# Optimization experiments

Measured on AMD Instinct MI355X. Metric: run time of the kernel, lower is better.

Reference implementation:

```python
import jax, jax.numpy as jnp
import numpy as np

B = 4096          # batch_size per view
D = 256           # projection feature dim
TEMP_F = 0.5      # temperature_f


def setup_inputs() -> dict:
    key = jax.random.key(0)
    k1, k2 = jax.random.split(key)
    return {
        "h_i": jax.random.normal(k1, (B, D), dtype=jnp.float32),
        "h_j": jax.random.normal(k2, (B, D), dtype=jnp.float32),
    }


def reference(h_i, h_j):
    # NT-Xent contrastive loss (forward_feature).
    batch = h_i.shape[0]
    N = 2 * batch
    h = jnp.concatenate([h_i, h_j], axis=0)                 # [N, D]
    sim = (h @ h.T) / TEMP_F                                # [N, N]

    # positives: sim(i, i+batch) and sim(i+batch, i)
    sim_i_j = jnp.diagonal(sim, offset=batch)               # [batch]
    sim_j_i = jnp.diagonal(sim, offset=-batch)              # [batch]
    pos = jnp.concatenate([sim_i_j, sim_j_i], axis=0)       # [N]

    # Torch builds logits = [pos_i, negatives_i] per row where negatives are
    # sim[i, :] with the diagonal AND the positive-pair entry removed, then
    # takes CE with label 0. Since the removed positive-pair entry equals
    # pos_i itself, logsumexp(logits_i) == logsumexp(sim[i, :] with only the
    # diagonal masked). So: loss_i = logsumexp(sim_masked[i]) - pos_i.
    neg_inf = jnp.finfo(sim.dtype).min
    eye = jnp.eye(N, dtype=bool)
    sim_masked = jnp.where(eye, neg_inf, sim)               # mask self-similarity
    lse = jax.nn.logsumexp(sim_masked, axis=1)              # [N]

    # CrossEntropyLoss(reduction='sum') / N  == mean over rows
    loss = jnp.mean(lse - pos)
    return loss
```

## Files before the change

kernel.cpp:

```cpp
#include <hip/hip_runtime.h>
#include <hip/hip_bf16.h>
#include <stdint.h>

#define BATCH 4096
#define N_TOT 8192
#define D_DIM 256
#define SHIFT 150.0f
#define SQRT2 1.41421356237309515f

typedef __bf16 bf16_t;
typedef bf16_t bf16x8 __attribute__((ext_vector_type(8)));
typedef bf16_t bf16x4 __attribute__((ext_vector_type(4)));
typedef float f32x4 __attribute__((ext_vector_type(4)));

__device__ __forceinline__ void gl_lds16(const void* g, void* l) {
  __builtin_amdgcn_global_load_lds(
      (const __attribute__((address_space(1))) void*)(uintptr_t)g,
      (__attribute__((address_space(3))) void*)(uint32_t)(uintptr_t)l,
      16, 0, 0);
}

__global__ void k_prep(const float* __restrict__ hi, const float* __restrict__ hj,
                       bf16_t* __restrict__ hb, float* __restrict__ Zrow,
                       float* __restrict__ posPartial) {
  const int wave = threadIdx.x >> 6, lane = threadIdx.x & 63;
  const int r = blockIdx.x * 4 + wave;
  const size_t off = (size_t)r * D_DIM + lane * 4;
  float4 a = *(const float4*)(hi + off);
  float4 b = *(const float4*)(hj + off);

  bf16x4 oa, ob;
  oa[0] = (bf16_t)(a.x * SQRT2); oa[1] = (bf16_t)(a.y * SQRT2);
  oa[2] = (bf16_t)(a.z * SQRT2); oa[3] = (bf16_t)(a.w * SQRT2);
  ob[0] = (bf16_t)(b.x * SQRT2); ob[1] = (bf16_t)(b.y * SQRT2);
  ob[2] = (bf16_t)(b.z * SQRT2); ob[3] = (bf16_t)(b.w * SQRT2);
  *(bf16x4*)(hb + off) = oa;
  *(bf16x4*)(hb + (size_t)BATCH * D_DIM + off) = ob;

  float d = a.x * b.x + a.y * b.y + a.z * b.z + a.w * b.w;
#pragma unroll
  for (int o = 32; o >= 1; o >>= 1) d += __shfl_xor(d, o);
  __shared__ float ps[4];
  if (lane == 0) ps[wave] = d;
  if (threadIdx.x < 8) Zrow[blockIdx.x * 8 + threadIdx.x] = 0.f;
  __syncthreads();
  if (threadIdx.x == 0) posPartial[blockIdx.x] = ps[0] + ps[1] + ps[2] + ps[3];
}

__global__ __launch_bounds__(256, 4) void k_gemm(const bf16_t* __restrict__ hb,
                                                 float* __restrict__ Zrow) {
  const int t = blockIdx.x;
  int bj = (int)((sqrtf(8.0f * (float)t + 1.0f) - 1.0f) * 0.5f);
  while ((bj + 1) * (bj + 2) / 2 <= t) ++bj;
  while (bj * (bj + 1) / 2 > t) --bj;
  const int bi = t - bj * (bj + 1) / 2;
  const int rBase = bi * 128;
  const int cBase = bj * 128;
  const bool diag = (bi == bj);

  __shared__ __align__(16) bf16_t As[128][64];
  __shared__ __align__(16) bf16_t Bs[128][64];
  const int tid = threadIdx.x;
  const int lane = tid & 63;
  const int wave = tid >> 6;

  const int half = wave & 1;
  const size_t stageRow = (size_t)((wave < 2 ? rBase : cBase) + half * 64);
  const int c_src = (lane & 7) ^ (lane >> 3);
  const bf16_t* gsrc = hb + stageRow * D_DIM + (size_t)(lane >> 3) * D_DIM + c_src * 8;
  bf16_t* lbase = (wave < 2) ? &As[half * 64][0] : &Bs[half * 64][0];

  const int wm = wave >> 1, wn = wave & 1;
  const int quad = lane >> 4, l16 = lane & 15;
  const int sw = l16 & 7;

  f32x4 acc[4][4];
#pragma unroll
  for (int i = 0; i < 4; ++i)
#pragma unroll
    for (int j = 0; j < 4; ++j) acc[i][j] = (f32x4){0.f, 0.f, 0.f, 0.f};

#pragma unroll
  for (int kc = 0; kc < 4; ++kc) {
    __syncthreads();
#pragma unroll
    for (int i = 0; i < 8; ++i)
      gl_lds16(gsrc + (size_t)i * 8 * D_DIM + kc * 64, lbase + i * 8 * 64);
    __syncthreads();
#pragma unroll
    for (int ks = 0; ks < 2; ++ks) {
      bf16x8 af[4], bfr[4];
      const int chunk = ((ks * 4 + quad) ^ sw) * 8;
#pragma unroll
      for (int mt = 0; mt < 4; ++mt)
        af[mt] = *(const bf16x8*)&As[wm * 64 + mt * 16 + l16][chunk];
#pragma unroll
      for (int nt = 0; nt < 4; ++nt)
        bfr[nt] = *(const bf16x8*)&Bs[wn * 64 + nt * 16 + l16][chunk];
#pragma unroll
      for (int mt = 0; mt < 4; ++mt)
#pragma unroll
        for (int nt = 0; nt < 4; ++nt)
          acc[mt][nt] = __builtin_amdgcn_mfma_f32_16x16x32_bf16(af[mt], bfr[nt],
                                                                acc[mt][nt], 0, 0, 0);
    }
  }

  const int rW = rBase + wm * 64 + quad * 4;
  const int cW = cBase + wn * 64 + l16;
  float colAcc[4] = {0.f, 0.f, 0.f, 0.f};
#pragma unroll
  for (int mt = 0; mt < 4; ++mt) {
#pragma unroll
    for (int rg = 0; rg < 4; ++rg) {
      const int rr = rW + mt * 16 + rg;
      float s = 0.f;
#pragma unroll
      for (int nt = 0; nt < 4; ++nt) {
        float e = __expf(acc[mt][nt][rg] - SHIFT);
        if (diag && (rr == cW + nt * 16)) e = 0.f;
        s += e;
        colAcc[nt] += e;
      }
      s += __shfl_xor(s, 1);
      s += __shfl_xor(s, 2);
      s += __shfl_xor(s, 4);
      s += __shfl_xor(s, 8);
      if (l16 == 0) atomicAdd(&Zrow[rr], s);
    }
  }
  if (!diag) {
#pragma unroll
    for (int nt = 0; nt < 4; ++nt) {
      float c = colAcc[nt];
      c += __shfl_xor(c, 16);
      c += __shfl_xor(c, 32);
      if (lane < 16) atomicAdd(&Zrow[cW + nt * 16], c);
    }
  }
}

__global__ void k_finish(const float* __restrict__ Zrow,
                         const float* __restrict__ posPartial,
                         float* __restrict__ out) {
  const int t = threadIdx.x;
  float4 z0 = *(const float4*)(Zrow + t * 8);
  float4 z1 = *(const float4*)(Zrow + t * 8 + 4);
  float sl = __logf(z0.x) + __logf(z0.y) + __logf(z0.z) + __logf(z0.w) +
             __logf(z1.x) + __logf(z1.y) + __logf(z1.z) + __logf(z1.w);
  float sp = posPartial[t];
#pragma unroll
  for (int o = 32; o >= 1; o >>= 1) {
    sl += __shfl_xor(sl, o);
    sp += __shfl_xor(sp, o);
  }
  __shared__ float pl[16], pp[16];
  const int wave = t >> 6, lane = t & 63;
  if (lane == 0) { pl[wave] = sl; pp[wave] = sp; }
  __syncthreads();
  if (t == 0) {
    float L = 0.f, P = 0.f;
    for (int i = 0; i < 16; ++i) { L += pl[i]; P += pp[i]; }
    out[0] = L / (float)N_TOT + SHIFT - P / 2048.0f;
  }
}

extern "C" void kernel_launch(void* const* d_in, const int* in_sizes, int n_in,
                              void* d_out, int out_size, void* d_ws, size_t ws_size,
                              hipStream_t stream) {
  const float* hi = (const float*)d_in[0];
  const float* hj = (const float*)d_in[1];
  float* out = (float*)d_out;

  bf16_t* hb = (bf16_t*)d_ws;
  float* Zrow = (float*)((char*)d_ws + (size_t)N_TOT * D_DIM * 2);
  float* posPartial = Zrow + N_TOT;

  k_prep<<<1024, 256, 0, stream>>>(hi, hj, hb, Zrow, posPartial);
  k_gemm<<<2080, 256, 0, stream>>>(hb, Zrow);
  k_finish<<<1, 1024, 0, stream>>>(Zrow, posPartial, out);
}
```

Measured before the change: 96.59 us.

## Double-buffer LDS tiles to overlap global loads with MFMA compute

Doubles the A/B LDS tiles and prefetches the next K-chunk into the alternate buffer while the current one is consumed, using manual vmcnt waits and raw barriers in place of paired __syncthreads. All fragments of a chunk are loaded before the MFMA burst, with a sched_barrier between. Launch bounds drop from 4 to 2 blocks per SM to allow more registers. Occupancy falls because of the doubled LDS (64KB per block) and the larger register budget, which may offset the latency hiding for a loop of only four K-chunks.

Result: slower. 103.2 us (+6.8%).

```diff
diff --git a/kernel.cpp b/kernel.cpp
--- a/kernel.cpp
+++ b/kernel.cpp
@@ -47,7 +47,7 @@
   if (threadIdx.x == 0) posPartial[blockIdx.x] = ps[0] + ps[1] + ps[2] + ps[3];
 }
 
-__global__ __launch_bounds__(256, 4) void k_gemm(const bf16_t* __restrict__ hb,
+__global__ __launch_bounds__(256, 2) void k_gemm(const bf16_t* __restrict__ hb,
                                                  float* __restrict__ Zrow) {
   const int t = blockIdx.x;
   int bj = (int)((sqrtf(8.0f * (float)t + 1.0f) - 1.0f) * 0.5f);
@@ -58,8 +58,8 @@
   const int cBase = bj * 128;
   const bool diag = (bi == bj);
 
-  __shared__ __align__(16) bf16_t As[128][64];
-  __shared__ __align__(16) bf16_t Bs[128][64];
+  __shared__ __align__(16) bf16_t As[2][128][64];
+  __shared__ __align__(16) bf16_t Bs[2][128][64];
   const int tid = threadIdx.x;
   const int lane = tid & 63;
   const int wave = tid >> 6;
@@ -68,7 +68,14 @@
   const size_t stageRow = (size_t)((wave < 2 ? rBase : cBase) + half * 64);
   const int c_src = (lane & 7) ^ (lane >> 3);
   const bf16_t* gsrc = hb + stageRow * D_DIM + (size_t)(lane >> 3) * D_DIM + c_src * 8;
-  bf16_t* lbase = (wave < 2) ? &As[half * 64][0] : &Bs[half * 64][0];
+  bf16_t* lbase = (wave < 2) ? &As[0][half * 64][0] : &Bs[0][half * 64][0];
+
+  auto STAGE = [&](int s, int b) {
+#pragma unroll
+    for (int i = 0; i < 8; ++i)
+      gl_lds16(gsrc + (size_t)i * 8 * D_DIM + s * 64,
+               lbase + b * (128 * 64) + i * 8 * 64);
+  };
 
   const int wm = wave >> 1, wn = wave & 1;
   const int quad = lane >> 4, l16 = lane & 15;
@@ -80,30 +87,43 @@
 #pragma unroll
     for (int j = 0; j < 4; ++j) acc[i][j] = (f32x4){0.f, 0.f, 0.f, 0.f};
 
-#pragma unroll
-  for (int kc = 0; kc < 4; ++kc) {
-    __syncthreads();
-#pragma unroll
-    for (int i = 0; i < 8; ++i)
-      gl_lds16(gsrc + (size_t)i * 8 * D_DIM + kc * 64, lbase + i * 8 * 64);
-    __syncthreads();
+  STAGE(0, 0);
+
+#pragma unroll
+  for (int k = 0; k < 4; ++k) {
+    const int b = k & 1;
+    if (k + 1 < 4) {
+      STAGE(k + 1, b ^ 1);
+      asm volatile("s_waitcnt vmcnt(8)" ::: "memory");
+    } else {
+      asm volatile("s_waitcnt vmcnt(0)" ::: "memory");
+    }
+    __builtin_amdgcn_s_barrier();
+
+    bf16x8 af[2][4], bfr[2][4];
 #pragma unroll
     for (int ks = 0; ks < 2; ++ks) {
-      bf16x8 af[4], bfr[4];
       const int chunk = ((ks * 4 + quad) ^ sw) * 8;
 #pragma unroll
       for (int mt = 0; mt < 4; ++mt)
-        af[mt] = *(const bf16x8*)&As[wm * 64 + mt * 16 + l16][chunk];
+        af[ks][mt] = *(const bf16x8*)&As[b][wm * 64 + mt * 16 + l16][chunk];
 #pragma unroll
       for (int nt = 0; nt < 4; ++nt)
-        bfr[nt] = *(const bf16x8*)&Bs[wn * 64 + nt * 16 + l16][chunk];
+        bfr[ks][nt] = *(const bf16x8*)&Bs[b][wn * 64 + nt * 16 + l16][chunk];
+    }
+    asm volatile("s_waitcnt lgkmcnt(0)" ::: "memory");
+    __builtin_amdgcn_sched_barrier(0);
+
+#pragma unroll
+    for (int ks = 0; ks < 2; ++ks)
 #pragma unroll
       for (int mt = 0; mt < 4; ++mt)
 #pragma unroll
         for (int nt = 0; nt < 4; ++nt)
-          acc[mt][nt] = __builtin_amdgcn_mfma_f32_16x16x32_bf16(af[mt], bfr[nt],
-                                                                acc[mt][nt], 0, 0, 0);
-    }
+          acc[mt][nt] = __builtin_amdgcn_mfma_f32_16x16x32_bf16(
+              af[ks][mt], bfr[ks][nt], acc[mt][nt], 0, 0, 0);
+
+    __builtin_amdgcn_s_barrier();
   }
 
   const int rW = rBase + wm * 64 + quad * 4;
```

## Drop LDS staging: plane-major bf16 layout with per-wave 64x64 tiles and register double-buffering

Applied to the files above, without the earlier changes.

The prep kernel now writes the bf16 features in a plane-major layout (8-element k-chunks per plane), so each lane can load MFMA fragments straight from global memory with coalesced 16-byte loads. The GEMM drops shared memory and block-wide barriers: each wave owns its own 64x64 upper-triangular tile and double-buffers fragments in registers, ordering the loads with manual vmcnt waits and scheduling fences. This removes LDS traffic and __syncthreads stalls, but every wave re-reads its operands from global/L2 with no reuse across waves, and the launch bound drops to 3 blocks per SIMD to make room for the extra registers.

After: 97.80 us. No clear change (+1.3%).

```diff
diff --git a/kernel.cpp b/kernel.cpp
--- a/kernel.cpp
+++ b/kernel.cpp
@@ -7,21 +7,19 @@
 #define D_DIM 256
 #define SHIFT 150.0f
 #define SQRT2 1.41421356237309515f
+#define NWTILE 8256
+#define PLANE 8192
 
 typedef __bf16 bf16_t;
 typedef bf16_t bf16x8 __attribute__((ext_vector_type(8)));
 typedef bf16_t bf16x4 __attribute__((ext_vector_type(4)));
 typedef float f32x4 __attribute__((ext_vector_type(4)));
 
-__device__ __forceinline__ void gl_lds16(const void* g, void* l) {
-  __builtin_amdgcn_global_load_lds(
-      (const __attribute__((address_space(1))) void*)(uintptr_t)g,
-      (__attribute__((address_space(3))) void*)(uint32_t)(uintptr_t)l,
-      16, 0, 0);
-}
+#define VMCNT(N) asm volatile("s_waitcnt vmcnt(" #N ")" ::: "memory")
+#define SCHED_FENCE() __builtin_amdgcn_sched_barrier(0)
 
 __global__ void k_prep(const float* __restrict__ hi, const float* __restrict__ hj,
-                       bf16_t* __restrict__ hb, float* __restrict__ Zrow,
+                       bf16_t* __restrict__ hbP, float* __restrict__ Zrow,
                        float* __restrict__ posPartial) {
   const int wave = threadIdx.x >> 6, lane = threadIdx.x & 63;
   const int r = blockIdx.x * 4 + wave;
@@ -34,8 +32,10 @@
   oa[2] = (bf16_t)(a.z * SQRT2); oa[3] = (bf16_t)(a.w * SQRT2);
   ob[0] = (bf16_t)(b.x * SQRT2); ob[1] = (bf16_t)(b.y * SQRT2);
   ob[2] = (bf16_t)(b.z * SQRT2); ob[3] = (bf16_t)(b.w * SQRT2);
-  *(bf16x4*)(hb + off) = oa;
-  *(bf16x4*)(hb + (size_t)BATCH * D_DIM + off) = ob;
+  const int plane = lane >> 1;
+  const int halfo = (lane & 1) * 4;
+  *(bf16x4*)(hbP + ((size_t)plane * PLANE + r) * 8 + halfo) = oa;
+  *(bf16x4*)(hbP + ((size_t)plane * PLANE + BATCH + r) * 8 + halfo) = ob;
 
   float d = a.x * b.x + a.y * b.y + a.z * b.z + a.w * b.w;
 #pragma unroll
@@ -47,32 +47,23 @@
   if (threadIdx.x == 0) posPartial[blockIdx.x] = ps[0] + ps[1] + ps[2] + ps[3];
 }
 
-__global__ __launch_bounds__(256, 4) void k_gemm(const bf16_t* __restrict__ hb,
+__global__ __launch_bounds__(256, 3) void k_gemm(const bf16_t* __restrict__ hbP,
                                                  float* __restrict__ Zrow) {
-  const int t = blockIdx.x;
+  const int lane = threadIdx.x & 63;
+  const int wave = threadIdx.x >> 6;
+  const int t = blockIdx.x * 4 + wave;
   int bj = (int)((sqrtf(8.0f * (float)t + 1.0f) - 1.0f) * 0.5f);
   while ((bj + 1) * (bj + 2) / 2 <= t) ++bj;
   while (bj * (bj + 1) / 2 > t) --bj;
   const int bi = t - bj * (bj + 1) / 2;
-  const int rBase = bi * 128;
-  const int cBase = bj * 128;
+  const int rBase = bi * 64;
+  const int cBase = bj * 64;
   const bool diag = (bi == bj);
 
-  __shared__ __align__(16) bf16_t As[128][64];
-  __shared__ __align__(16) bf16_t Bs[128][64];
-  const int tid = threadIdx.x;
-  const int lane = tid & 63;
-  const int wave = tid >> 6;
+  const int quad = lane >> 4, l16 = lane & 15;
 
-  const int half = wave & 1;
-  const size_t stageRow = (size_t)((wave < 2 ? rBase : cBase) + half * 64);
-  const int c_src = (lane & 7) ^ (lane >> 3);
-  const bf16_t* gsrc = hb + stageRow * D_DIM + (size_t)(lane >> 3) * D_DIM + c_src * 8;
-  bf16_t* lbase = (wave < 2) ? &As[half * 64][0] : &Bs[half * 64][0];
-
-  const int wm = wave >> 1, wn = wave & 1;
-  const int quad = lane >> 4, l16 = lane & 15;
-  const int sw = l16 & 7;
+  const bf16_t* aP = hbP + ((size_t)quad * PLANE + rBase + l16) * 8;
+  const bf16_t* bP = hbP + ((size_t)quad * PLANE + cBase + l16) * 8;
 
   f32x4 acc[4][4];
 #pragma unroll
@@ -80,34 +71,37 @@
 #pragma unroll
     for (int j = 0; j < 4; ++j) acc[i][j] = (f32x4){0.f, 0.f, 0.f, 0.f};
 
+  auto LOADS = [&](bf16x8 A[4], bf16x8 B[4], int ks) {
 #pragma unroll
-  for (int kc = 0; kc < 4; ++kc) {
-    __syncthreads();
+    for (int mt = 0; mt < 4; ++mt)
+      A[mt] = *(const bf16x8*)(aP + (size_t)ks * (4 * PLANE * 8) + mt * 128);
 #pragma unroll
-    for (int i = 0; i < 8; ++i)
-      gl_lds16(gsrc + (size_t)i * 8 * D_DIM + kc * 64, lbase + i * 8 * 64);
-    __syncthreads();
+    for (int nt = 0; nt < 4; ++nt)
+      B[nt] = *(const bf16x8*)(bP + (size_t)ks * (4 * PLANE * 8) + nt * 128);
+  };
+  auto MM = [&](const bf16x8 A[4], const bf16x8 B[4]) {
 #pragma unroll
-    for (int ks = 0; ks < 2; ++ks) {
-      bf16x8 af[4], bfr[4];
-      const int chunk = ((ks * 4 + quad) ^ sw) * 8;
-#pragma unroll
-      for (int mt = 0; mt < 4; ++mt)
-        af[mt] = *(const bf16x8*)&As[wm * 64 + mt * 16 + l16][chunk];
+    for (int mt = 0; mt < 4; ++mt)
 #pragma unroll
       for (int nt = 0; nt < 4; ++nt)
-        bfr[nt] = *(const bf16x8*)&Bs[wn * 64 + nt * 16 + l16][chunk];
-#pragma unroll
-      for (int mt = 0; mt < 4; ++mt)
-#pragma unroll
-        for (int nt = 0; nt < 4; ++nt)
-          acc[mt][nt] = __builtin_amdgcn_mfma_f32_16x16x32_bf16(af[mt], bfr[nt],
-                                                                acc[mt][nt], 0, 0, 0);
-    }
-  }
+        acc[mt][nt] = __builtin_amdgcn_mfma_f32_16x16x32_bf16(A[mt], B[nt],
+                                                              acc[mt][nt], 0, 0, 0);
+  };
 
-  const int rW = rBase + wm * 64 + quad * 4;
-  const int cW = cBase + wn * 64 + l16;
+  bf16x8 aX[4], bX[4], aY[4], bY[4];
+  LOADS(aX, bX, 0);
+  LOADS(aY, bY, 1);
+  VMCNT(8); SCHED_FENCE(); MM(aX, bX); LOADS(aX, bX, 2);
+  VMCNT(8); SCHED_FENCE(); MM(aY, bY); LOADS(aY, bY, 3);
+  VMCNT(8); SCHED_FENCE(); MM(aX, bX); LOADS(aX, bX, 4);
+  VMCNT(8); SCHED_FENCE(); MM(aY, bY); LOADS(aY, bY, 5);
+  VMCNT(8); SCHED_FENCE(); MM(aX, bX); LOADS(aX, bX, 6);
+  VMCNT(8); SCHED_FENCE(); MM(aY, bY); LOADS(aY, bY, 7);
+  VMCNT(8); SCHED_FENCE(); MM(aX, bX);
+  VMCNT(0); SCHED_FENCE(); MM(aY, bY);
+
+  const int rW = rBase + quad * 4;
+  const int cW = cBase + l16;
   float colAcc[4] = {0.f, 0.f, 0.f, 0.f};
 #pragma unroll
   for (int mt = 0; mt < 4; ++mt) {
@@ -172,11 +166,11 @@
   const float* hj = (const float*)d_in[1];
   float* out = (float*)d_out;
 
-  bf16_t* hb = (bf16_t*)d_ws;
+  bf16_t* hbP = (bf16_t*)d_ws;
   float* Zrow = (float*)((char*)d_ws + (size_t)N_TOT * D_DIM * 2);
   float* posPartial = Zrow + N_TOT;
 
-  k_prep<<<1024, 256, 0, stream>>>(hi, hj, hb, Zrow, posPartial);
-  k_gemm<<<2080, 256, 0, stream>>>(hb, Zrow);
+  k_prep<<<1024, 256, 0, stream>>>(hi, hj, hbP, Zrow, posPartial);
+  k_gemm<<<NWTILE / 4, 256, 0, stream>>>(hbP, Zrow);
   k_finish<<<1, 1024, 0, stream>>>(Zrow, posPartial, out);
 }
```
